# Optimization experiments

Hardware: AMD Instinct MI355X
Metric: run time of the kernel (lower is better)

## Reference

```python
import jax, jax.numpy as jnp
from jax import lax
import numpy as np

TAU_R = 1.0
TAU_W = 5.0
W_MIN, W_MAX = 0.0, 0.05
N_MBON, N_FBN, N_DAN, N_KC = 20, 60, 20, 200
N_RECUR = N_MBON + N_FBN + N_DAN
B, T = 256, 61


def setup_inputs() -> dict:
    key = jax.random.key(0)
    ks = jax.random.split(key, 8)
    r_kc = jax.random.uniform(ks[0], (B, N_KC, T), dtype=jnp.float32)
    r_ext = jax.random.uniform(ks[1], (B, 2, T), dtype=jnp.float32)
    time = jnp.arange(T, dtype=jnp.float32) * 0.5  # dt = 0.5
    # KC->MBON plastic weights start at the max value (0.05), as in init
    W0_W = jax.random.uniform(ks[2], (B, N_MBON, N_KC), dtype=jnp.float32) * W_MAX
    W0_w = jax.random.uniform(ks[3], (B, N_MBON, N_KC), dtype=jnp.float32) * W_MAX
    sqrt2 = np.sqrt(2.0)
    W_mbon = jax.random.normal(ks[4], (N_RECUR, N_MBON)) * np.sqrt(1.0 / (sqrt2 * N_MBON))
    W_fbn = jax.random.normal(ks[5], (N_RECUR, N_FBN)) * np.sqrt(1.0 / (sqrt2 * N_FBN))
    W_dan = jax.random.normal(ks[6], (N_RECUR, N_DAN)) * np.sqrt(1.0 / (sqrt2 * N_DAN))
    W_recur = jnp.concatenate([W_mbon, W_fbn, W_dan], axis=1).astype(jnp.float32)
    W_ext = jax.random.normal(ks[7], (N_FBN, 2), dtype=jnp.float32)
    bias = jnp.full((N_RECUR,), 0.1, dtype=jnp.float32)
    W_readout = jax.random.normal(jax.random.fold_in(key, 99), (1, N_MBON), dtype=jnp.float32) / np.sqrt(N_MBON)
    return {"r_kc": r_kc, "r_ext": r_ext, "time": time, "n_batch": B,
            "W0_W": W0_W, "W0_w": W0_w, "W_recur": W_recur, "W_ext": W_ext,
            "bias": bias, "W_readout": W_readout}


def reference(r_kc, r_ext, time, n_batch, W0_W, W0_w, W_recur, W_ext, bias, W_readout):
    n_mbon, n_kc = W0_W.shape[1], W0_W.shape[2]
    n_fbn = W_ext.shape[0]
    n_recur = W_recur.shape[0]
    n_dan = n_recur - n_mbon - n_fbn
    nb = r_kc.shape[0]
    dt = time[1] - time[0]

    # initial state: FBN/DAN at 0.1, MBON at 0
    r_init = jnp.full((nb, n_recur), 0.1, dtype=r_kc.dtype).at[:, :n_mbon].set(0.0)
    # DAN->MBON weights are zeroed
    Wr = W_recur.at[:n_mbon, -n_dan:].set(0.0)
    rbk0 = r_kc[:, :, 0]            # KC eligibility trace
    rbd0 = r_init[:, -n_dan:]       # DAN eligibility trace
    readout0 = jnp.einsum('om,bm->bo', W_readout, r_init[:, :n_mbon]).squeeze(-1)
    zeros_dan = jnp.zeros((nb, n_dan), dtype=r_kc.dtype)

    def step(carry, xs):
        r, W, wt, rbk, rbd = carry
        rk_t, re_t = xs                                   # [B,n_kc], [B,n_ext]
        I_kc = jnp.einsum('bmk,bk->bm', W, rk_t)          # KC -> MBON via plastic W
        I_fbn = jnp.einsum('fe,be->bf', W_ext, re_t)      # context -> FBN
        I_tot = jnp.concatenate([I_kc, I_fbn, zeros_dan], axis=1)
        Wr_prod = jnp.einsum('sr,br->bs', Wr, r)
        dr = (-r + jax.nn.relu(Wr_prod + bias + I_tot)) / TAU_R
        r_new = r + dr * dt
        # plasticity update (uses the *new* DAN activity)
        rbk_new = rbk + (rk_t - rbk) * dt / TAU_W
        r_dan = r_new[:, -n_dan:]
        rbd_new = rbd + (r_dan - rbd) * dt / TAU_W
        dw = (jnp.einsum('bd,bk->bdk', rbd_new, rk_t)
              - jnp.einsum('bd,bk->bdk', r_dan, rbk_new))
        wt_new = wt + dw * dt
        W_new = jnp.clip(W + (-W + wt_new) / TAU_W * dt, W_MIN, W_MAX)
        ro = jnp.einsum('om,bm->bo', W_readout, r_new[:, :n_mbon]).squeeze(-1)
        return (r_new, W_new, wt_new, rbk_new, rbd_new), (r_new, W_new, wt_new, ro)

    xs = (jnp.moveaxis(r_kc, 2, 0)[:-1], jnp.moveaxis(r_ext, 2, 0)[:-1])
    carry0 = (r_init, W0_W, W0_w, rbk0, rbd0)
    _, (r_s, W_s, wt_s, ro_s) = lax.scan(step, carry0, xs)
    r_series = jnp.concatenate([r_init[None], r_s], axis=0)    # [T,B,n_recur]
    W_series = jnp.concatenate([W0_W[None], W_s], axis=0)      # [T,B,n_mbon,n_kc]
    wt_series = jnp.concatenate([W0_w[None], wt_s], axis=0)    # [T,B,n_mbon,n_kc]
    readout = jnp.concatenate([readout0[None], ro_s], axis=0)  # [T,B]
    return r_series, W_series, wt_series, readout
```

## Files before the change

### kernel.cpp

```cpp
#include <hip/hip_runtime.h>


#define NKC   200
#define NREC  100
#define TSTEP 61
#define NSTEP 60
#define PSTR  52
#define NTHR  512

typedef float vfloat4 __attribute__((ext_vector_type(4)));

__device__ __forceinline__ void bar_lds() {
    __builtin_amdgcn_sched_barrier(0);
    asm volatile("s_waitcnt lgkmcnt(0)");
    __builtin_amdgcn_s_barrier();
    __builtin_amdgcn_sched_barrier(0);
}

__device__ __forceinline__ void nt_store4(float* p, float4 v) {
    vfloat4 t;
    t.x = v.x; t.y = v.y; t.z = v.z; t.w = v.w;
    __builtin_nontemporal_store(t, (vfloat4*)p);
}
__device__ __forceinline__ void nt_store1(float* p, float v) {
    __builtin_nontemporal_store(v, p);
}

__global__ __launch_bounds__(NTHR, 1) void cond_rnn_kernel(
    const float* __restrict__ r_kc, const float* __restrict__ r_ext,
    const float* __restrict__ timev, const float* __restrict__ W0_W,
    const float* __restrict__ W0_w, const float* __restrict__ W_recur,
    const float* __restrict__ W_ext, const float* __restrict__ bias,
    const float* __restrict__ W_readout, float* __restrict__ out, int B)
{
    int b = blockIdx.x;
    if ((B & 7) == 0) {
        const int cpx = B >> 3;
        b = (blockIdx.x & 7) * cpx + (blockIdx.x >> 3);
    }
    const int tid = threadIdx.x;
    const float dt  = timev[1] - timev[0];
    const float dtw = dt / 5.0f;

    __shared__ __align__(16) float s_rk[TSTEP * NKC];
    __shared__ __align__(16) float s_re[128];
    __shared__ __align__(16) float s_Wro[32];
    __shared__ __align__(16) float s_r[2][112];
    __shared__ __align__(16) float s_rbd[32];
    __shared__ __align__(16) float s_part[20 * PSTR];

    const float* rk_b = r_kc + (size_t)b * (NKC * TSTEP);
    for (int f = tid; f < NKC * TSTEP; f += NTHR) {
        int k = f / TSTEP, t = f - k * TSTEP;
        s_rk[t * NKC + k] = rk_b[f];
    }
    const float* re_b = r_ext + (size_t)b * (2 * TSTEP);
    if (tid < 2 * TSTEP) s_re[tid] = re_b[tid];

    float4 wrreg[25];
    if (tid < 100) {
        const float* wrow = W_recur + tid * NREC;
        #pragma unroll
        for (int j4 = 0; j4 < 25; ++j4)
            wrreg[j4] = *(const float4*)(wrow + 4 * j4);
        if (tid < 20) {
            #pragma unroll
            for (int j4 = 20; j4 < 25; ++j4) {
                wrreg[j4].x = 0.f; wrreg[j4].y = 0.f;
                wrreg[j4].z = 0.f; wrreg[j4].w = 0.f;
            }
        }
    }

    if (tid < 20)  s_Wro[tid] = W_readout[tid];
    if (tid < 100) s_r[0][tid] = (tid < 20) ? 0.f : 0.1f;
    if (tid < 20)  s_rbd[tid] = 0.1f;

    float my_bias = 0.f, we0 = 0.f, we1 = 0.f;
    if (tid < 100) my_bias = bias[tid];
    if (tid >= 20 && tid < 80) { we0 = W_ext[(tid - 20) * 2]; we1 = W_ext[(tid - 20) * 2 + 1]; }
    float rbd_mine = 0.1f;
    float r_mine   = (tid < 20) ? 0.f : 0.1f;

    float* out_r  = out;
    float* out_W  = out + (size_t)TSTEP * B * 100;
    float* out_wt = out_W + (size_t)TSTEP * B * 4000;
    float* out_ro = out_wt + (size_t)TSTEP * B * 4000;

    float4 Wreg[2], wtreg[2], rbkreg[2], rkc[2];
    const float* W0Wb = W0_W + (size_t)b * 4000;
    const float* W0wb = W0_w + (size_t)b * 4000;
    #pragma unroll
    for (int i = 0; i < 2; ++i) {
        int c = tid + NTHR * i;
        if (c < 1000) {
            Wreg[i]  = *(const float4*)(W0Wb + 4 * c);
            wtreg[i] = *(const float4*)(W0wb + 4 * c);
            nt_store4(out_W  + (size_t)b * 4000 + 4 * c, Wreg[i]);
            nt_store4(out_wt + (size_t)b * 4000 + 4 * c, wtreg[i]);
        }
    }
    if (tid < 100) nt_store1(out_r + (size_t)b * 100 + tid, r_mine);

    __syncthreads();

    #pragma unroll
    for (int i = 0; i < 2; ++i) {
        int c = tid + NTHR * i;
        if (c < 1000) {
            int k0 = (4 * c) % NKC;
            int m  = c / 50;
            float4 rk0 = *(const float4*)(s_rk + k0);
            rbkreg[i] = rk0;
            rkc[i]    = rk0;
            float4 w = Wreg[i];
            s_part[m * PSTR + (c % 50)] =
                w.x * rk0.x + w.y * rk0.y + w.z * rk0.z + w.w * rk0.w;
        }
    }
    if (tid == 255) {
        float ro = 0.f;
        #pragma unroll
        for (int mm = 0; mm < 20; ++mm) ro += s_Wro[mm] * s_r[0][mm];
        nt_store1(out_ro + b, ro);
    }
    __syncthreads();

    for (int it = 0; it < NSTEP; ++it) {
        const int cur = it & 1, nxt = cur ^ 1;

        if (tid < 100) {
            float acc = my_bias;
            if (tid < 20) {
                const float* pp = s_part + tid * PSTR;
                #pragma unroll
                for (int q4 = 0; q4 < 12; ++q4) {
                    float4 p4 = *(const float4*)(pp + 4 * q4);
                    acc += p4.x + p4.y + p4.z + p4.w;
                }
                acc += pp[48] + pp[49];
            } else if (tid < 80) {
                acc = fmaf(we0, s_re[it], acc);
                acc = fmaf(we1, s_re[TSTEP + it], acc);
            }
            #pragma unroll
            for (int j4 = 0; j4 < 25; ++j4) {
                float4 w4 = wrreg[j4];
                float4 r4 = *(const float4*)(&s_r[cur][4 * j4]);
                acc = fmaf(w4.x, r4.x, acc); acc = fmaf(w4.y, r4.y, acc);
                acc = fmaf(w4.z, r4.z, acc); acc = fmaf(w4.w, r4.w, acc);
            }
            float drive = acc > 0.f ? acc : 0.f;
            float rn = r_mine + dt * (drive - r_mine);
            r_mine = rn;
            s_r[nxt][tid] = rn;
            nt_store1(out_r + (size_t)(it + 1) * B * 100 + (size_t)b * 100 + tid, rn);
            if (tid >= 80) {
                rbd_mine += (rn - rbd_mine) * dtw;
                s_rbd[tid - 80] = rbd_mine;
            }
        }
        bar_lds();

        float* oW  = out_W  + (size_t)(it + 1) * B * 4000 + (size_t)b * 4000;
        float* owt = out_wt + (size_t)(it + 1) * B * 4000 + (size_t)b * 4000;
        const float* rk_nx  = s_rk + (it + 1) * NKC;
        #pragma unroll
        for (int i = 0; i < 2; ++i) {
            int c = tid + NTHR * i;
            if (c < 1000) {
                int k0 = (4 * c) % NKC;
                int m  = c / 50;
                float4 rk4 = rkc[i];
                float4 rkn = *(const float4*)(rk_nx + k0);
                rkc[i] = rkn;
                float rbdn = s_rbd[m];
                float rdan = s_r[nxt][80 + m];
                float4 rb = rbkreg[i];
                rb.x += (rk4.x - rb.x) * dtw;  rb.y += (rk4.y - rb.y) * dtw;
                rb.z += (rk4.z - rb.z) * dtw;  rb.w += (rk4.w - rb.w) * dtw;
                rbkreg[i] = rb;
                float4 wt = wtreg[i];
                wt.x = fmaf(rbdn * rk4.x - rdan * rb.x, dt, wt.x);
                wt.y = fmaf(rbdn * rk4.y - rdan * rb.y, dt, wt.y);
                wt.z = fmaf(rbdn * rk4.z - rdan * rb.z, dt, wt.z);
                wt.w = fmaf(rbdn * rk4.w - rdan * rb.w, dt, wt.w);
                wtreg[i] = wt;
                float4 w = Wreg[i];
                w.x += (wt.x - w.x) * dtw;  w.y += (wt.y - w.y) * dtw;
                w.z += (wt.z - w.z) * dtw;  w.w += (wt.w - w.w) * dtw;
                w.x = fminf(fmaxf(w.x, 0.f), 0.05f);
                w.y = fminf(fmaxf(w.y, 0.f), 0.05f);
                w.z = fminf(fmaxf(w.z, 0.f), 0.05f);
                w.w = fminf(fmaxf(w.w, 0.f), 0.05f);
                Wreg[i] = w;
                s_part[m * PSTR + (c % 50)] =
                    w.x * rkn.x + w.y * rkn.y + w.z * rkn.z + w.w * rkn.w;
                nt_store4(owt + 4 * c, wt);
                nt_store4(oW  + 4 * c, w);
            }
        }
        if (tid == 255) {
            float ro = 0.f;
            #pragma unroll
            for (int mm = 0; mm < 20; ++mm) ro += s_Wro[mm] * s_r[nxt][mm];
            nt_store1(out_ro + (size_t)(it + 1) * B + b, ro);
        }
        bar_lds();
    }
}

extern "C" void kernel_launch(void* const* d_in, const int* in_sizes, int n_in,
                              void* d_out, int out_size, void* d_ws, size_t ws_size,
                              hipStream_t stream) {
    const float* r_kc      = (const float*)d_in[0];
    const float* r_ext     = (const float*)d_in[1];
    const float* timev     = (const float*)d_in[2];
    const float* W0_W      = (const float*)d_in[4];
    const float* W0_w      = (const float*)d_in[5];
    const float* W_recur   = (const float*)d_in[6];
    const float* W_ext     = (const float*)d_in[7];
    const float* bias      = (const float*)d_in[8];
    const float* W_readout = (const float*)d_in[9];

    const int B = in_sizes[0] / (NKC * TSTEP);
    cond_rnn_kernel<<<dim3(B), dim3(NTHR), 0, stream>>>(
        r_kc, r_ext, timev, W0_W, W0_w, W_recur, W_ext, bias, W_readout,
        (float*)d_out, B);
}
```

Baseline: 516.0 us.

## Split recurrent state and weight-series output into two kernels via workspace

The single kernel becomes two. The first runs the recurrent dynamics and keeps W in registers only to compute the MBON drive. It writes the transposed KC rates and per-step DAN rates and traces to a workspace. A second kernel with twice as many blocks at 2 blocks per CU replays the elementwise W/wt update and streams the large W and wt series to memory. The goal is to take the heavy output stores off the serial recurrence path and spread them across more parallel blocks, at the cost of a second launch, workspace traffic and the update arithmetic being done twice.

After: 605.2 us. +17.3%, slower.

```diff
diff --git a/kernel.cpp b/kernel.cpp
--- a/kernel.cpp
+++ b/kernel.cpp
@@ -26,18 +26,34 @@
     __builtin_nontemporal_store(v, p);
 }
 
-__global__ __launch_bounds__(NTHR, 1) void cond_rnn_kernel(
+__device__ __forceinline__ void elem_update(
+    const float4 rk4, const float rbdn, const float rdan,
+    const float dt, const float dtw,
+    float4& rb, float4& wt, float4& w)
+{
+    rb.x += (rk4.x - rb.x) * dtw;  rb.y += (rk4.y - rb.y) * dtw;
+    rb.z += (rk4.z - rb.z) * dtw;  rb.w += (rk4.w - rb.w) * dtw;
+    wt.x = fmaf(rbdn * rk4.x - rdan * rb.x, dt, wt.x);
+    wt.y = fmaf(rbdn * rk4.y - rdan * rb.y, dt, wt.y);
+    wt.z = fmaf(rbdn * rk4.z - rdan * rb.z, dt, wt.z);
+    wt.w = fmaf(rbdn * rk4.w - rdan * rb.w, dt, wt.w);
+    w.x += (wt.x - w.x) * dtw;  w.y += (wt.y - w.y) * dtw;
+    w.z += (wt.z - w.z) * dtw;  w.w += (wt.w - w.w) * dtw;
+    w.x = fminf(fmaxf(w.x, 0.f), 0.05f);
+    w.y = fminf(fmaxf(w.y, 0.f), 0.05f);
+    w.z = fminf(fmaxf(w.z, 0.f), 0.05f);
+    w.w = fminf(fmaxf(w.w, 0.f), 0.05f);
+}
+
+__global__ __launch_bounds__(NTHR, 1) void rnn_state_kernel(
     const float* __restrict__ r_kc, const float* __restrict__ r_ext,
     const float* __restrict__ timev, const float* __restrict__ W0_W,
     const float* __restrict__ W0_w, const float* __restrict__ W_recur,
     const float* __restrict__ W_ext, const float* __restrict__ bias,
-    const float* __restrict__ W_readout, float* __restrict__ out, int B)
+    const float* __restrict__ W_readout, float* __restrict__ out,
+    float* __restrict__ rkT, float* __restrict__ aux, int B)
 {
-    int b = blockIdx.x;
-    if ((B & 7) == 0) {
-        const int cpx = B >> 3;
-        b = (blockIdx.x & 7) * cpx + (blockIdx.x >> 3);
-    }
+    const int b   = blockIdx.x;
     const int tid = threadIdx.x;
     const float dt  = timev[1] - timev[0];
     const float dtw = dt / 5.0f;
@@ -96,13 +112,17 @@
         if (c < 1000) {
             Wreg[i]  = *(const float4*)(W0Wb + 4 * c);
             wtreg[i] = *(const float4*)(W0wb + 4 * c);
-            nt_store4(out_W  + (size_t)b * 4000 + 4 * c, Wreg[i]);
-            nt_store4(out_wt + (size_t)b * 4000 + 4 * c, wtreg[i]);
         }
     }
     if (tid < 100) nt_store1(out_r + (size_t)b * 100 + tid, r_mine);
 
     __syncthreads();
+
+    float* rkT_b = rkT + (size_t)b * (TSTEP * NKC);
+    for (int f4 = tid; f4 < (TSTEP * NKC) / 4; f4 += NTHR) {
+        float4 v = *(const float4*)(s_rk + 4 * f4);
+        nt_store4(rkT_b + 4 * f4, v);
+    }
 
     #pragma unroll
     for (int i = 0; i < 2; ++i) {
@@ -125,6 +145,8 @@
         nt_store1(out_ro + b, ro);
     }
     __syncthreads();
+
+    float* aux_b = aux + (size_t)b * (NSTEP * 40);
 
     for (int it = 0; it < NSTEP; ++it) {
         const int cur = it & 1, nxt = cur ^ 1;
@@ -158,13 +180,13 @@
             if (tid >= 80) {
                 rbd_mine += (rn - rbd_mine) * dtw;
                 s_rbd[tid - 80] = rbd_mine;
+                nt_store1(aux_b + it * 40 + (tid - 80), rn);
+                nt_store1(aux_b + it * 40 + 20 + (tid - 80), rbd_mine);
             }
         }
         bar_lds();
 
-        float* oW  = out_W  + (size_t)(it + 1) * B * 4000 + (size_t)b * 4000;
-        float* owt = out_wt + (size_t)(it + 1) * B * 4000 + (size_t)b * 4000;
-        const float* rk_nx  = s_rk + (it + 1) * NKC;
+        const float* rk_nx = s_rk + (it + 1) * NKC;
         #pragma unroll
         for (int i = 0; i < 2; ++i) {
             int c = tid + NTHR * i;
@@ -176,28 +198,10 @@
                 rkc[i] = rkn;
                 float rbdn = s_rbd[m];
                 float rdan = s_r[nxt][80 + m];
-                float4 rb = rbkreg[i];
-                rb.x += (rk4.x - rb.x) * dtw;  rb.y += (rk4.y - rb.y) * dtw;
-                rb.z += (rk4.z - rb.z) * dtw;  rb.w += (rk4.w - rb.w) * dtw;
-                rbkreg[i] = rb;
-                float4 wt = wtreg[i];
-                wt.x = fmaf(rbdn * rk4.x - rdan * rb.x, dt, wt.x);
-                wt.y = fmaf(rbdn * rk4.y - rdan * rb.y, dt, wt.y);
-                wt.z = fmaf(rbdn * rk4.z - rdan * rb.z, dt, wt.z);
-                wt.w = fmaf(rbdn * rk4.w - rdan * rb.w, dt, wt.w);
-                wtreg[i] = wt;
+                elem_update(rk4, rbdn, rdan, dt, dtw, rbkreg[i], wtreg[i], Wreg[i]);
                 float4 w = Wreg[i];
-                w.x += (wt.x - w.x) * dtw;  w.y += (wt.y - w.y) * dtw;
-                w.z += (wt.z - w.z) * dtw;  w.w += (wt.w - w.w) * dtw;
-                w.x = fminf(fmaxf(w.x, 0.f), 0.05f);
-                w.y = fminf(fmaxf(w.y, 0.f), 0.05f);
-                w.z = fminf(fmaxf(w.z, 0.f), 0.05f);
-                w.w = fminf(fmaxf(w.w, 0.f), 0.05f);
-                Wreg[i] = w;
                 s_part[m * PSTR + (c % 50)] =
                     w.x * rkn.x + w.y * rkn.y + w.z * rkn.z + w.w * rkn.w;
-                nt_store4(owt + 4 * c, wt);
-                nt_store4(oW  + 4 * c, w);
             }
         }
         if (tid == 255) {
@@ -207,6 +211,62 @@
             nt_store1(out_ro + (size_t)(it + 1) * B + b, ro);
         }
         bar_lds();
+    }
+}
+
+__global__ __launch_bounds__(NTHR, 2) void w_series_kernel(
+    const float* __restrict__ W0_W, const float* __restrict__ W0_w,
+    const float* __restrict__ timev,
+    const float* __restrict__ rkT, const float* __restrict__ aux,
+    float* __restrict__ out, int B)
+{
+    const int b    = blockIdx.x >> 1;
+    const int half = blockIdx.x & 1;
+    const int tid  = threadIdx.x;
+    const float dt  = timev[1] - timev[0];
+    const float dtw = dt / 5.0f;
+
+    __shared__ __align__(16) float s_rk[TSTEP * NKC];
+    __shared__ __align__(16) float s_aux[NSTEP * 40];
+
+    const float* rkT_b = rkT + (size_t)b * (TSTEP * NKC);
+    for (int f4 = tid; f4 < (TSTEP * NKC) / 4; f4 += NTHR)
+        *(float4*)(s_rk + 4 * f4) = *(const float4*)(rkT_b + 4 * f4);
+    const float* aux_b = aux + (size_t)b * (NSTEP * 40);
+    for (int f4 = tid; f4 < (NSTEP * 40) / 4; f4 += NTHR)
+        *(float4*)(s_aux + 4 * f4) = *(const float4*)(aux_b + 4 * f4);
+
+    float* out_W  = out + (size_t)TSTEP * B * 100;
+    float* out_wt = out_W + (size_t)TSTEP * B * 4000;
+
+    const bool active = (tid < 500);
+    const int  c = half * 500 + tid;
+
+    float4 w, wt, rb, rkc;
+    if (active) {
+        w  = *(const float4*)(W0_W + (size_t)b * 4000 + 4 * c);
+        wt = *(const float4*)(W0_w + (size_t)b * 4000 + 4 * c);
+        nt_store4(out_W  + (size_t)b * 4000 + 4 * c, w);
+        nt_store4(out_wt + (size_t)b * 4000 + 4 * c, wt);
+    }
+    __syncthreads();
+    if (!active) return;
+
+    const int k0 = (4 * c) % NKC;
+    const int m  = c / 50;
+    rkc = *(const float4*)(s_rk + k0);
+    rb  = rkc;
+
+    for (int it = 0; it < NSTEP; ++it) {
+        float4 rkn = *(const float4*)(s_rk + (it + 1) * NKC + k0);
+        float rdan = s_aux[it * 40 + m];
+        float rbdn = s_aux[it * 40 + 20 + m];
+        elem_update(rkc, rbdn, rdan, dt, dtw, rb, wt, w);
+        rkc = rkn;
+        float* oW  = out_W  + (size_t)(it + 1) * B * 4000 + (size_t)b * 4000;
+        float* owt = out_wt + (size_t)(it + 1) * B * 4000 + (size_t)b * 4000;
+        nt_store4(owt + 4 * c, wt);
+        nt_store4(oW  + 4 * c, w);
     }
 }
 
@@ -224,7 +284,13 @@
     const float* W_readout = (const float*)d_in[9];
 
     const int B = in_sizes[0] / (NKC * TSTEP);
-    cond_rnn_kernel<<<dim3(B), dim3(NTHR), 0, stream>>>(
+    float* ws  = (float*)d_ws;
+    float* rkT = ws;
+    float* aux = ws + (size_t)B * (TSTEP * NKC);
+
+    rnn_state_kernel<<<dim3(B), dim3(NTHR), 0, stream>>>(
         r_kc, r_ext, timev, W0_W, W0_w, W_recur, W_ext, bias, W_readout,
-        (float*)d_out, B);
-}
+        (float*)d_out, rkT, aux, B);
+    w_series_kernel<<<dim3(2 * B), dim3(NTHR), 0, stream>>>(
+        W0_W, W0_w, timev, rkT, aux, (float*)d_out, B);
+}
```
